# Optimization experiments

Measured on AMD Instinct MI355X. Metric: run time of the kernel, lower is better.

Reference implementation:

```python
import jax, jax.numpy as jnp
import numpy as np

N = 200000      # nodes
E = 1600000     # edges
B = 1000        # graphs
SD = 64         # state_dim
AD = 32         # action_dim
H = 128         # HIDDEN_LAYER
EPS = 1e-5


def setup_inputs() -> dict:
    key = jax.random.key(0)
    ks = jax.random.split(key, 16)
    x = jax.random.normal(ks[0], (N, SD), dtype=jnp.float32)
    action = jax.random.normal(ks[1], (N, AD), dtype=jnp.float32)
    edge_index = jax.random.randint(ks[2], (2, E), 0, N, dtype=jnp.int64)
    batch_size = jnp.sort(jax.random.randint(ks[3], (N,), 0, B, dtype=jnp.int64))
    # parameters (Linear weights stored [in, out]; torch init std=0.1 for fc layers)
    W_gcn = jax.random.normal(ks[4], (SD, H), dtype=jnp.float32) / np.sqrt(SD)
    b_gcn = jnp.zeros((H,), jnp.float32)
    g0 = jnp.ones((H,), jnp.float32); be0 = jnp.zeros((H,), jnp.float32)
    W1 = jax.random.normal(ks[5], (H, H), dtype=jnp.float32) * 0.1
    b1 = jnp.zeros((H,), jnp.float32)
    g1 = jnp.ones((H,), jnp.float32); be1 = jnp.zeros((H,), jnp.float32)
    W2 = jax.random.normal(ks[6], (AD, H), dtype=jnp.float32) * 0.1
    b2 = jnp.zeros((H,), jnp.float32)
    g2 = jnp.ones((H,), jnp.float32); be2 = jnp.zeros((H,), jnp.float32)
    W3 = jax.random.normal(ks[7], (2 * H, 1), dtype=jnp.float32) * 0.1
    b3 = jnp.zeros((1,), jnp.float32)
    return dict(x=x, action=action, W_gcn=W_gcn, b_gcn=b_gcn, g0=g0, be0=be0,
                W1=W1, b1=b1, g1=g1, be1=be1, W2=W2, b2=b2, g2=g2, be2=be2,
                W3=W3, b3=b3, edge_index=edge_index, batch_size=batch_size)


def _bn(h, gamma, beta):
    # BatchNorm1d, training-mode batch statistics over the node axis
    mu = jnp.mean(h, axis=0)
    var = jnp.var(h, axis=0)
    return (h - mu) * jax.lax.rsqrt(var + EPS) * gamma + beta


def _gcn(x, edge_index, W, b):
    # GCN conv with self-loops and symmetric normalization:
    # out_i = sum_{j in N(i) u {i}} (d_i d_j)^{-1/2} (x_j W) + b
    loops = jnp.arange(N, dtype=edge_index.dtype)
    src = jnp.concatenate([edge_index[0], loops])
    dst = jnp.concatenate([edge_index[1], loops])
    deg = jax.ops.segment_sum(jnp.ones_like(dst, dtype=x.dtype), dst, num_segments=N)
    dinv = jax.lax.rsqrt(deg)                       # deg >= 1 due to self-loops
    norm = dinv[src] * dinv[dst]                    # [E+N]
    xw = x @ W                                      # [N, H]
    msg = xw[src] * norm[:, None]                   # [E+N, H]
    return jax.ops.segment_sum(msg, dst, num_segments=N) + b


def reference(x, action, W_gcn, b_gcn, g0, be0, W1, b1, g1, be1,
              W2, b2, g2, be2, W3, b3, edge_index, batch_size):
    h0 = jax.nn.relu(_gcn(x, edge_index, W_gcn, b_gcn))
    h0n = _bn(h0, g0, be0)
    h1 = jax.nn.relu(h0n @ W1 + b1)
    h1n = _bn(h1, g1, be1)
    h2 = jax.nn.relu(action @ W2 + b2)
    h2n = _bn(h2, g2, be2)
    feat = jnp.concatenate([h1n, h2n], axis=1)      # [N, 2H]
    sums = jax.ops.segment_sum(feat, batch_size, num_segments=B)
    cnts = jax.ops.segment_sum(jnp.ones((N,), feat.dtype), batch_size, num_segments=B)
    pooled = sums / jnp.maximum(cnts, 1.0)[:, None]  # [B, 2H]
    return pooled @ W3 + b3                          # [B, 1]
```

## Files before the change

kernel.cpp:

```cpp
#include <hip/hip_runtime.h>

typedef unsigned short u16;
typedef unsigned int   u32;
typedef __bf16 bf16x8 __attribute__((ext_vector_type(8)));
typedef float  f32x4  __attribute__((ext_vector_type(4)));

#define EPS 1e-5f
#define BSHIFT 9

__device__ __forceinline__ float b2f(u16 u){ union{u32 i; float f;} v; v.i=((u32)u)<<16; return v.f; }
__device__ __forceinline__ u16 f2b(float f){
  u32 x = __float_as_uint(f);
  u32 r = x + 0x7fffu + ((x>>16)&1u);
  return (u16)(r>>16);
}

template<int K, bool RELU, bool HASBIAS, bool AF32, bool POOL>
__global__ __launch_bounds__(256) void k_gemm(const void* __restrict__ Av,
                                              const u16* __restrict__ BhiT,
                                              const u16* __restrict__ BloT,
                                              const float* __restrict__ bias,
                                              u16* __restrict__ C,
                                              float* __restrict__ stats,
                                              const int* __restrict__ batch,
                                              float* __restrict__ P, int M)
{
  constexpr int KM = K / 8;
  constexpr int KR = K / 32;
  __shared__ u16 lds[2 * 64 * K];
  __shared__ float sred[64], qred[64];
  const int tid = threadIdx.x;
  const int halfg = gridDim.x >> 1;
  const int ch = (blockIdx.x >= halfg) ? 1 : 0;
  const int t0 = blockIdx.x - ch * halfg;
  for (int i = tid; i < 64 * KM; i += 256) {
    const int n = i / KM, kb = i % KM;
    const int kb2 = kb ^ (n & (KM - 1));
    const int gsrc = ((ch * 64 + n) * KM + kb) * 8;
    *(uint4*)(&lds[(n * KM + kb2) * 8])          = *(const uint4*)(BhiT + gsrc);
    *(uint4*)(&lds[64 * K + (n * KM + kb2) * 8]) = *(const uint4*)(BloT + gsrc);
  }
  if (tid < 64) { sred[tid] = 0.f; qred[tid] = 0.f; }
  __syncthreads();
  const int wid = tid >> 6, lane = tid & 63, q = lane >> 4, r16 = lane & 15;
  const int nmt = (M + 127) >> 7;
  float ls[4], lq[4];
#pragma unroll
  for (int nb = 0; nb < 4; nb++) { ls[nb] = 0.f; lq[nb] = 0.f; }
  float bv[4];
#pragma unroll
  for (int nb = 0; nb < 4; nb++) bv[nb] = HASBIAS ? bias[ch * 64 + nb * 16 + r16] : 0.f;

  for (int mt = t0; mt < nmt; mt += halfg) {
    const int row0 = mt << 7;
    const bool ok1 = (row0 + 64) < M;

    bf16x8 av[2][KR];
    if (AF32) {
      const float* Af = (const float*)Av + (size_t)(row0 + (wid << 4) + r16) * K + q * 8;
#pragma unroll
      for (int kk = 0; kk < KR; kk++) {
        f32x4 x0 = *(const f32x4*)(Af + kk * 32);
        f32x4 x1 = *(const f32x4*)(Af + kk * 32 + 4);
#pragma unroll
        for (int j = 0; j < 4; j++) { av[0][kk][j] = (__bf16)x0[j]; av[0][kk][4 + j] = (__bf16)x1[j]; }
      }
      if (ok1) {
        const float* Ag = Af + (size_t)64 * K;
#pragma unroll
        for (int kk = 0; kk < KR; kk++) {
          f32x4 x0 = *(const f32x4*)(Ag + kk * 32);
          f32x4 x1 = *(const f32x4*)(Ag + kk * 32 + 4);
#pragma unroll
          for (int j = 0; j < 4; j++) { av[1][kk][j] = (__bf16)x0[j]; av[1][kk][4 + j] = (__bf16)x1[j]; }
        }
      }
    } else {
      const u16* Ab = (const u16*)Av + (size_t)(row0 + (wid << 4) + r16) * K + q * 8;
#pragma unroll
      for (int kk = 0; kk < KR; kk++) av[0][kk] = *(const bf16x8*)(Ab + kk * 32);
      if (ok1) {
#pragma unroll
        for (int kk = 0; kk < KR; kk++) av[1][kk] = *(const bf16x8*)(Ab + (size_t)64 * K + kk * 32);
      }
    }

    f32x4 acc[2][4];
#pragma unroll
    for (int rt = 0; rt < 2; rt++)
#pragma unroll
      for (int nb = 0; nb < 4; nb++) acc[rt][nb] = (f32x4){0.f, 0.f, 0.f, 0.f};
#pragma unroll
    for (int kk = 0; kk < KR; kk++) {
#pragma unroll
      for (int nb = 0; nb < 4; nb++) {
        const int n = nb * 16 + r16;
        const int kb2 = (kk * 4 + q) ^ (n & (KM - 1));
        const bf16x8 bh = *(const bf16x8*)(&lds[(n * KM + kb2) * 8]);
        const bf16x8 bl = *(const bf16x8*)(&lds[64 * K + (n * KM + kb2) * 8]);
        acc[0][nb] = __builtin_amdgcn_mfma_f32_16x16x32_bf16(av[0][kk], bh, acc[0][nb], 0, 0, 0);
        acc[0][nb] = __builtin_amdgcn_mfma_f32_16x16x32_bf16(av[0][kk], bl, acc[0][nb], 0, 0, 0);
        if (ok1) {
          acc[1][nb] = __builtin_amdgcn_mfma_f32_16x16x32_bf16(av[1][kk], bh, acc[1][nb], 0, 0, 0);
          acc[1][nb] = __builtin_amdgcn_mfma_f32_16x16x32_bf16(av[1][kk], bl, acc[1][nb], 0, 0, 0);
        }
      }
    }

#pragma unroll
    for (int rt = 0; rt < 2; rt++) {
      if (rt && !ok1) continue;
      const int rbase = row0 + rt * 64 + (wid << 4) + (q << 2);
#pragma unroll
      for (int nb = 0; nb < 4; nb++) {
        const int col = ch * 64 + nb * 16 + r16;
#pragma unroll
        for (int r = 0; r < 4; r++) {
          float v = acc[rt][nb][r] + bv[nb];
          if (RELU) v = fmaxf(v, 0.f);
          ls[nb] += v; lq[nb] += v * v;
          if (!POOL) C[(size_t)(rbase + r) * 128 + col] = f2b(v);
          else acc[rt][nb][r] = v;
        }
      }
      if (POOL) {
        int bg[4];
#pragma unroll
        for (int r = 0; r < 4; r++) bg[r] = batch[rbase + r];
        const int g0 = __shfl(bg[0], 0, 64);
        const int g1 = __shfl(bg[3], 48, 64);
        for (int g = g0; g <= g1; ++g) {
#pragma unroll
          for (int nb = 0; nb < 4; nb++) {
            float sv = 0.f;
#pragma unroll
            for (int r = 0; r < 4; r++) sv += (bg[r] == g) ? acc[rt][nb][r] : 0.f;
            sv += __shfl_xor(sv, 16, 64);
            sv += __shfl_xor(sv, 32, 64);
            if (q == 0) atomicAdd(&P[g * 128 + ch * 64 + nb * 16 + r16], sv);
          }
        }
      }
    }
  }
#pragma unroll
  for (int nb = 0; nb < 4; nb++) {
    atomicAdd(&sred[nb * 16 + r16], ls[nb]);
    atomicAdd(&qred[nb * 16 + r16], lq[nb]);
  }
  __syncthreads();
  if (tid < 64) {
    atomicAdd(&stats[ch * 64 + tid], sred[tid]);
    atomicAdd(&stats[128 + ch * 64 + tid], qred[tid]);
  }
}

__global__ void k_prep0(const float* __restrict__ Wg, const float* __restrict__ W2,
                        u16* __restrict__ WghiT, u16* __restrict__ WgloT,
                        u16* __restrict__ W2hiT, u16* __restrict__ W2loT,
                        const int* __restrict__ batch, int* __restrict__ gofs,
                        int* __restrict__ zbase, int zwords, int NZ, int N, int B)
{
  const int bid = blockIdx.x, t = threadIdx.x;
  if (bid < NZ) {
    const int i = bid * 2048 + t * 8;
    if (i < zwords) {
      *(int4*)(zbase + i)     = make_int4(0, 0, 0, 0);
      *(int4*)(zbase + i + 4) = make_int4(0, 0, 0, 0);
    }
  } else if (bid < NZ + 48) {
    const int i = (bid - NZ) * 256 + t;
    if (i < 64 * 128) {
      int k = i >> 7, n = i & 127;
      float w = Wg[i]; u16 h = f2b(w);
      WghiT[n * 64 + k] = h; WgloT[n * 64 + k] = f2b(w - b2f(h));
    } else if (i < 64 * 128 + 32 * 128) {
      int j = i - 64 * 128;
      int k = j >> 7, n = j & 127;
      float w = W2[j]; u16 h = f2b(w);
      W2hiT[n * 32 + k] = h; W2loT[n * 32 + k] = f2b(w - b2f(h));
    }
  } else {
    const int i = (bid - NZ - 48) * 256 + t;
    if (i == 0) { for (int g = 0; g <= batch[0]; g++) gofs[g] = 0; }
    if (i == N - 1) { for (int g = batch[N - 1] + 1; g <= B; g++) gofs[g] = N; }
    if (i < N - 1) {
      const int b0 = batch[i], b1 = batch[i + 1];
      for (int g = b0 + 1; g <= b1; g++) gofs[g] = i + 1;
    }
  }
}

__global__ __launch_bounds__(256) void k_bincnt(const int* __restrict__ dst, int* __restrict__ btot,
                                                int E, int NB)
{
  extern __shared__ int hist[];
  const int tid = threadIdx.x;
  for (int i = tid; i < NB; i += 256) hist[i] = 0;
  __syncthreads();
  const int chunk = (E + gridDim.x - 1) / gridDim.x;
  const int start = blockIdx.x * chunk;
  const int end = min(start + chunk, E);
  for (int e = start + tid; e < end; e += 256) atomicAdd(&hist[((u32)dst[e]) >> BSHIFT], 1);
  __syncthreads();
  for (int i = tid; i < NB; i += 256) if (hist[i]) atomicAdd(&btot[i], hist[i]);
}

__global__ void k_exscan(const int* __restrict__ in, int* __restrict__ out, int n)
{
  __shared__ int s[256];
  const int t = threadIdx.x;
  const int per = (n + 255) / 256;
  const int base = t * per;
  int loc[8]; int sum = 0;
  for (int j = 0; j < per; j++) { int v = (base + j < n) ? in[base + j] : 0; loc[j] = sum; sum += v; }
  s[t] = sum; __syncthreads();
  for (int o = 1; o < 256; o <<= 1) {
    int x = (t >= o) ? s[t - o] : 0;
    __syncthreads();
    s[t] += x;
    __syncthreads();
  }
  const int ex = s[t] - sum;
  for (int j = 0; j < per; j++) if (base + j < n) out[base + j] = ex + loc[j];
  if (t == 255) out[n] = s[255];
}

__global__ __launch_bounds__(256) void k_bin(const int* __restrict__ src, const int* __restrict__ dst,
                                             const int* __restrict__ bbase, int* __restrict__ bcur,
                                             uint2* __restrict__ pairs, int E, int NB)
{
  extern __shared__ int lds[];
  int* hist = lds; int* wbase = lds + NB;
  const int tid = threadIdx.x;
  for (int i = tid; i < NB; i += 256) hist[i] = 0;
  __syncthreads();
  const int chunk = (E + gridDim.x - 1) / gridDim.x;
  const int start = blockIdx.x * chunk;
  const int end = min(start + chunk, E);
  for (int e = start + tid; e < end; e += 256) atomicAdd(&hist[((u32)dst[e]) >> BSHIFT], 1);
  __syncthreads();
  for (int i = tid; i < NB; i += 256) {
    int c = hist[i];
    wbase[i] = c ? bbase[i] + atomicAdd(&bcur[i], c) : 0;
    hist[i] = 0;
  }
  __syncthreads();
  for (int e = start + tid; e < end; e += 256) {
    const int d = dst[e];
    const int b = ((u32)d) >> BSHIFT;
    const int o = atomicAdd(&hist[b], 1);
    pairs[wbase[b] + o] = make_uint2((u32)d, (u32)src[e]);
  }
}

__global__ __launch_bounds__(256) void k_bucket(const uint2* __restrict__ pairs,
                                                const int* __restrict__ bbase,
                                                const float* __restrict__ x,
                                                int* __restrict__ offsets, float* __restrict__ dinv,
                                                int* __restrict__ elist, u16* __restrict__ y,
                                                int N, int NB, int Etot)
{
  __shared__ int hist[512];
  __shared__ int scan[256];
  __shared__ int lcur[512];
  __shared__ float sdinv[512];
  const int b = blockIdx.x, t = threadIdx.x;
  const int nbase = b << BSHIFT;
  const int nn = min(1 << BSHIFT, N - nbase);
  hist[t] = 0; hist[256 + t] = 0;
  __syncthreads();
  const int p0 = bbase[b], p1 = bbase[b + 1];
  for (int p = p0 + t; p < p1; p += 256) atomicAdd(&hist[pairs[p].x - nbase], 1);
  __syncthreads();
  const int h0 = hist[2 * t], h1 = hist[2 * t + 1];
  const int psum = h0 + h1;
  scan[t] = psum; __syncthreads();
  for (int o = 1; o < 256; o <<= 1) {
    int xx = (t >= o) ? scan[t - o] : 0;
    __syncthreads();
    scan[t] += xx;
    __syncthreads();
  }
  const int ex = scan[t] - psum;
  const int li0 = 2 * t, li1 = 2 * t + 1;
  if (li0 < nn) {
    const int i = nbase + li0;
    const int off = p0 + ex + i;
    const float d = rsqrtf((float)(h0 + 1));
    offsets[i] = off; elist[off] = i; lcur[li0] = off + 1;
    dinv[i] = d; sdinv[li0] = d;
  }
  if (li1 < nn) {
    const int i = nbase + li1;
    const int off = p0 + ex + h0 + i;
    const float d = rsqrtf((float)(h1 + 1));
    offsets[i] = off; elist[off] = i; lcur[li1] = off + 1;
    dinv[i] = d; sdinv[li1] = d;
  }
  if (b == NB - 1 && t == 0) offsets[N] = Etot;
  __syncthreads();
  for (int p = p0 + t; p < p1; p += 256) {
    const uint2 pr = pairs[p];
    const int pos = atomicAdd(&lcur[pr.x - nbase], 1);
    elist[pos] = (int)pr.y;
  }
  const size_t ebase = (size_t)nbase * 64;
  const int total = nn * 64;
  for (int i = t * 8; i < total; i += 256 * 8) {
    const float d = sdinv[i >> 6];
    f32x4 a = *(const f32x4*)(x + ebase + i);
    f32x4 c = *(const f32x4*)(x + ebase + i + 4);
    u16 o[8];
#pragma unroll
    for (int j = 0; j < 4; j++) { o[j] = f2b(a[j] * d); o[4 + j] = f2b(c[j] * d); }
    *(uint4*)(y + ebase + i) = *(uint4*)o;
  }
}

__global__ __launch_bounds__(256) void k_agg(const u16* __restrict__ y, const int* __restrict__ offsets,
                                             const int* __restrict__ elist, const float* __restrict__ dinv,
                                             u16* __restrict__ aggx, int n)
{
  const int lane = threadIdx.x & 63;
  const int half = lane >> 5, l32 = lane & 31;
  const int g4 = l32 >> 3, sub = lane & 7;
  const int wid  = (blockIdx.x * 256 + threadIdx.x) >> 6;
  const int nw   = gridDim.x * 4;
  const int npair = (n + 1) >> 1;
  for (int pr = wid; pr < npair; pr += nw) {
    const int node = pr * 2 + half;
    const int s0 = offsets[node], s1 = offsets[node + 1];
    const int mydeg = s1 - s0;
    const int degA = __shfl(mydeg, 0, 64);
    const int degB = __shfl(mydeg, 32, 64);
    const int degmax = max(degA, degB);
    float a[8];
#pragma unroll
    for (int t = 0; t < 8; t++) a[t] = 0.f;
    for (int base = 0; base < degmax; base += 32) {
      const int m = mydeg - base;
      const int ev = (base + l32 < mydeg) ? elist[s0 + base + l32] : 0;
      const int iters = (min(32, degmax - base) + 3) >> 2;
      for (int it = 0; it < iters; it++) {
        const int j = it * 4 + g4;
        const int idx = __shfl(ev, half * 32 + j, 64);
        if (j < m) {
          const uint4 v = *(const uint4*)(y + (size_t)idx * 64 + sub * 8);
          const u32 w[4] = {v.x, v.y, v.z, v.w};
#pragma unroll
          for (int t = 0; t < 4; t++) {
            a[2 * t]     += b2f((u16)w[t]);
            a[2 * t + 1] += b2f((u16)(w[t] >> 16));
          }
        }
      }
    }
#pragma unroll
    for (int t = 0; t < 8; t++) {
      a[t] += __shfl_xor(a[t], 8, 64);
      a[t] += __shfl_xor(a[t], 16, 64);
    }
    if (g4 == 0) {
      const float di = dinv[node];
      u16 o[8];
#pragma unroll
      for (int t = 0; t < 8; t++) o[t] = f2b(a[t] * di);
      *(uint4*)(aggx + (size_t)node * 64 + sub * 8) = *(uint4*)o;
    }
  }
}

__global__ void k_prep1(const float* __restrict__ stats0, const float* __restrict__ W1,
                        const float* __restrict__ b1, const float* __restrict__ g0,
                        const float* __restrict__ be0, u16* __restrict__ W1hiT,
                        u16* __restrict__ W1loT, float* __restrict__ b1p, float n)
{
  __shared__ float A[8], Csh[8];
  const int t = threadIdx.x;
  if (t < 8) {
    const int k = blockIdx.x * 8 + t;
    const float mu = stats0[k] / n;
    const float var = fmaxf(stats0[128 + k] / n - mu * mu, 0.f);
    const float a = g0[k] * rsqrtf(var + EPS);
    A[t] = a; Csh[t] = be0[k] - mu * a;
  }
  __syncthreads();
  float acc = (blockIdx.x == 0) ? b1[t] : 0.f;
#pragma unroll
  for (int kk = 0; kk < 8; kk++) {
    const int k = blockIdx.x * 8 + kk;
    const float w0 = W1[k * 128 + t];
    acc += Csh[kk] * w0;
    const float w = A[kk] * w0;
    const u16 h = f2b(w);
    W1hiT[t * 128 + k] = h;
    W1loT[t * 128 + k] = f2b(w - b2f(h));
  }
  atomicAdd(&b1p[t], acc);
}

__global__ void k_prep2(const float* __restrict__ stats1, const float* __restrict__ stats2,
                        const float* __restrict__ g1, const float* __restrict__ be1,
                        const float* __restrict__ g2, const float* __restrict__ be2,
                        const float* __restrict__ W3, const float* __restrict__ b3,
                        float* __restrict__ w1f, float* __restrict__ w2f,
                        float* __restrict__ constS, float n)
{
  __shared__ float red[256];
  const int t = threadIdx.x;
  float c, wv;
  if (t < 128) {
    const float mu = stats1[t] / n;
    const float var = fmaxf(stats1[128 + t] / n - mu * mu, 0.f);
    const float a = g1[t] * rsqrtf(var + EPS);
    c = be1[t] - mu * a;
    wv = W3[t];
    w1f[t] = a * wv;
  } else {
    const int f = t - 128;
    const float mu = stats2[f] / n;
    const float var = fmaxf(stats2[128 + f] / n - mu * mu, 0.f);
    const float a = g2[f] * rsqrtf(var + EPS);
    c = be2[f] - mu * a;
    wv = W3[t];
    w2f[f] = a * wv;
  }
  red[t] = c * wv; __syncthreads();
  for (int o = 128; o; o >>= 1) { if (t < o) red[t] += red[t + o]; __syncthreads(); }
  if (t == 0) { constS[0] = red[0] + b3[0]; constS[1] = b3[0]; }
}

__global__ void k_out2(const float* __restrict__ P1, const float* __restrict__ P2,
                       const int* __restrict__ gofs, const float* __restrict__ w1f,
                       const float* __restrict__ w2f, const float* __restrict__ constS,
                       float* __restrict__ out, int B)
{
  const int lane = threadIdx.x & 63;
  const int g = (blockIdx.x * 256 + threadIdx.x) >> 6;
  if (g >= B) return;
  const int c = gofs[g + 1] - gofs[g];
  const int k = 2 * lane;
  float d = P1[g * 128 + k] * w1f[k] + P1[g * 128 + k + 1] * w1f[k + 1]
          + P2[g * 128 + k] * w2f[k] + P2[g * 128 + k + 1] * w2f[k + 1];
#pragma unroll
  for (int o = 1; o < 64; o <<= 1) d += __shfl_xor(d, o, 64);
  if (lane == 0) out[g] = (c > 0) ? d / (float)c + constS[0] : constS[1];
}

extern "C" void kernel_launch(void* const* d_in, const int* in_sizes, int n_in,
                              void* d_out, int out_size, void* d_ws, size_t ws_size,
                              hipStream_t stream)
{
  const float* x    = (const float*)d_in[0];
  const float* act  = (const float*)d_in[1];
  const float* Wg   = (const float*)d_in[2];
  const float* bg   = (const float*)d_in[3];
  const float* g0   = (const float*)d_in[4];
  const float* be0  = (const float*)d_in[5];
  const float* W1   = (const float*)d_in[6];
  const float* b1   = (const float*)d_in[7];
  const float* g1   = (const float*)d_in[8];
  const float* be1  = (const float*)d_in[9];
  const float* W2   = (const float*)d_in[10];
  const float* b2   = (const float*)d_in[11];
  const float* g2   = (const float*)d_in[12];
  const float* be2  = (const float*)d_in[13];
  const float* W3   = (const float*)d_in[14];
  const float* b3   = (const float*)d_in[15];
  const int* eidx   = (const int*)d_in[16];
  const int* batch  = (const int*)d_in[17];

  const int N = in_sizes[17];
  const int E = in_sizes[16] / 2;
  const int B = out_size;
  const int* src = eidx;
  const int* dst = eidx + E;
  const int NB = (N + (1 << BSHIFT) - 1) >> BSHIFT;

  char* ws = (char*)d_ws;
  size_t off = 0;
  auto alloc = [&](size_t bytes) -> char* {
    off = (off + 255) & ~(size_t)255;
    char* p = ws + off; off += bytes; return p;
  };

  u16* bufA = (u16*)alloc((size_t)N * 128 * 2);
  u16* xb   = (u16*)alloc((size_t)N * 64 * 2);
  u16* aggx = (u16*)alloc((size_t)N * 64 * 2);

  int zwords = 768 + 128 + 2 * NB + 2 * 128 * B;
  zwords = (zwords + 7) & ~7;
  char* zbase   = alloc((size_t)zwords * 4);
  float* stats0 = (float*)zbase;
  float* stats1 = stats0 + 256;
  float* stats2 = stats1 + 256;
  float* b1p    = stats2 + 256;
  int*   btot   = (int*)(b1p + 128);
  int*   bcur   = btot + NB;
  float* P1     = (float*)(bcur + NB);
  float* P2     = P1 + 128 * B;

  int*   offsets = (int*)alloc((size_t)(N + 1) * 4);
  float* dinv    = (float*)alloc((size_t)N * 4);
  int*   elist   = (int*)alloc((size_t)(E + N) * 4);
  uint2* pairs   = (uint2*)alloc((size_t)E * 8);
  int*   bbase   = (int*)alloc((size_t)(NB + 1) * 4);
  int*   gofs    = (int*)alloc((size_t)(B + 1) * 4);
  u16*   WghiT   = (u16*)alloc(128 * 64 * 2);
  u16*   WgloT   = (u16*)alloc(128 * 64 * 2);
  u16*   W1hiT   = (u16*)alloc(128 * 128 * 2);
  u16*   W1loT   = (u16*)alloc(128 * 128 * 2);
  u16*   W2hiT   = (u16*)alloc(128 * 32 * 2);
  u16*   W2loT   = (u16*)alloc(128 * 32 * 2);
  float* w1f     = (float*)alloc(128 * 4);
  float* w2f     = (float*)alloc(128 * 4);
  float* constS  = (float*)alloc(2 * 4);

  u16* h0 = bufA;

  const int NZ = (zwords + 2047) / 2048;
  const int nbounds = (N + 255) / 256;
  k_prep0<<<NZ + 48 + nbounds, 256, 0, stream>>>(Wg, W2, WghiT, WgloT, W2hiT, W2loT,
                                                 batch, gofs, (int*)zbase, zwords, NZ, N, B);
  k_bincnt<<<256, 256, NB * 4, stream>>>(dst, btot, E, NB);
  k_exscan<<<1, 256, 0, stream>>>(btot, bbase, NB);
  k_bin<<<256, 256, 2 * NB * 4, stream>>>(src, dst, bbase, bcur, pairs, E, NB);
  k_bucket<<<NB, 256, 0, stream>>>(pairs, bbase, x, offsets, dinv, elist, xb, N, NB, E + N);
  k_agg<<<2048, 256, 0, stream>>>(xb, offsets, elist, dinv, aggx, N);
  k_gemm<64, true, true, false, false><<<1024, 256, 0, stream>>>(aggx, WghiT, WgloT, bg,
                                                                 h0, stats0, nullptr, nullptr, N);
  k_prep1<<<16, 128, 0, stream>>>(stats0, W1, b1, g0, be0, W1hiT, W1loT, b1p, (float)N);
  k_gemm<128, true, true, false, true><<<1024, 256, 0, stream>>>(h0, W1hiT, W1loT, b1p,
                                                                 nullptr, stats1, batch, P1, N);
  k_gemm<32, true, true, true, true><<<1024, 256, 0, stream>>>(act, W2hiT, W2loT, b2,
                                                               nullptr, stats2, batch, P2, N);
  k_prep2<<<1, 256, 0, stream>>>(stats1, stats2, g1, be1, g2, be2, W3, b3, w1f, w2f, constS, (float)N);
  k_out2<<<(B * 64 + 255) / 256, 256, 0, stream>>>(P1, P2, gofs, w1f, w2f, constS, (float*)d_out, B);
}
```

Before: 397.1 us.

## Merge the two pooling GEMMs into one launch and fuse prep2 into output

Moves the GEMM body into a device function that uses dynamic shared memory, so a combined kernel can run the K=128 hidden GEMM and the K=32 action GEMM as disjoint block ranges of a single launch. It also folds the BatchNorm-to-W3 folding kernel into the final output kernel, which recomputes the scale factors per block in shared memory. Grid sizes change from 1024 to 768 and 512 blocks. This removes two launches and lets the two independent GEMMs share the GPU. In exchange the K=32 blocks reserve the larger K=128 shared-memory size, which may limit occupancy, and every output block repeats the small reduction.

```diff
diff --git a/kernel.cpp b/kernel.cpp
--- a/kernel.cpp
+++ b/kernel.cpp
@@ -16,23 +16,25 @@
 }
 
 template<int K, bool RELU, bool HASBIAS, bool AF32, bool POOL>
-__global__ __launch_bounds__(256) void k_gemm(const void* __restrict__ Av,
-                                              const u16* __restrict__ BhiT,
-                                              const u16* __restrict__ BloT,
-                                              const float* __restrict__ bias,
-                                              u16* __restrict__ C,
-                                              float* __restrict__ stats,
-                                              const int* __restrict__ batch,
-                                              float* __restrict__ P, int M)
+__device__ __forceinline__ void gemm_body(const void* __restrict__ Av,
+                                          const u16* __restrict__ BhiT,
+                                          const u16* __restrict__ BloT,
+                                          const float* __restrict__ bias,
+                                          u16* __restrict__ C,
+                                          float* __restrict__ stats,
+                                          const int* __restrict__ batch,
+                                          float* __restrict__ P, int M,
+                                          int bid, int halfg)
 {
   constexpr int KM = K / 8;
   constexpr int KR = K / 32;
-  __shared__ u16 lds[2 * 64 * K];
-  __shared__ float sred[64], qred[64];
+  extern __shared__ char smem[];
+  u16* lds    = (u16*)smem;
+  float* sred = (float*)(smem + (size_t)2 * 64 * K * 2);
+  float* qred = sred + 64;
   const int tid = threadIdx.x;
-  const int halfg = gridDim.x >> 1;
-  const int ch = (blockIdx.x >= halfg) ? 1 : 0;
-  const int t0 = blockIdx.x - ch * halfg;
+  const int ch = (bid >= halfg) ? 1 : 0;
+  const int t0 = bid - ch * halfg;
   for (int i = tid; i < 64 * KM; i += 256) {
     const int n = i / KM, kb = i % KM;
     const int kb2 = kb ^ (n & (KM - 1));
@@ -153,6 +155,43 @@
     atomicAdd(&stats[ch * 64 + tid], sred[tid]);
     atomicAdd(&stats[128 + ch * 64 + tid], qred[tid]);
   }
+}
+
+template<int K, bool RELU, bool HASBIAS, bool AF32, bool POOL>
+__global__ __launch_bounds__(256) void k_gemm(const void* __restrict__ Av,
+                                              const u16* __restrict__ BhiT,
+                                              const u16* __restrict__ BloT,
+                                              const float* __restrict__ bias,
+                                              u16* __restrict__ C,
+                                              float* __restrict__ stats,
+                                              const int* __restrict__ batch,
+                                              float* __restrict__ P, int M)
+{
+  gemm_body<K, RELU, HASBIAS, AF32, POOL>(Av, BhiT, BloT, bias, C, stats, batch, P, M,
+                                          blockIdx.x, gridDim.x >> 1);
+}
+
+__global__ __launch_bounds__(256) void k_gemm2(const void* __restrict__ A1,
+                                               const u16* __restrict__ B1hi,
+                                               const u16* __restrict__ B1lo,
+                                               const float* __restrict__ bias1,
+                                               float* __restrict__ stats1,
+                                               float* __restrict__ P1,
+                                               const void* __restrict__ A2,
+                                               const u16* __restrict__ B2hi,
+                                               const u16* __restrict__ B2lo,
+                                               const float* __restrict__ bias2,
+                                               float* __restrict__ stats2,
+                                               float* __restrict__ P2,
+                                               const int* __restrict__ batch,
+                                               int M, int g1blk, int g2blk)
+{
+  if ((int)blockIdx.x < g1blk)
+    gemm_body<128, true, true, false, true>(A1, B1hi, B1lo, bias1, nullptr, stats1,
+                                            batch, P1, M, blockIdx.x, g1blk >> 1);
+  else
+    gemm_body<32, true, true, true, true>(A2, B2hi, B2lo, bias2, nullptr, stats2,
+                                          batch, P2, M, blockIdx.x - g1blk, g2blk >> 1);
 }
 
 __global__ void k_prep0(const float* __restrict__ Wg, const float* __restrict__ W2,
@@ -400,14 +439,15 @@
   atomicAdd(&b1p[t], acc);
 }
 
-__global__ void k_prep2(const float* __restrict__ stats1, const float* __restrict__ stats2,
-                        const float* __restrict__ g1, const float* __restrict__ be1,
-                        const float* __restrict__ g2, const float* __restrict__ be2,
-                        const float* __restrict__ W3, const float* __restrict__ b3,
-                        float* __restrict__ w1f, float* __restrict__ w2f,
-                        float* __restrict__ constS, float n)
-{
-  __shared__ float red[256];
+__global__ void k_out3(const float* __restrict__ P1, const float* __restrict__ P2,
+                       const int* __restrict__ gofs,
+                       const float* __restrict__ stats1, const float* __restrict__ stats2,
+                       const float* __restrict__ g1, const float* __restrict__ be1,
+                       const float* __restrict__ g2, const float* __restrict__ be2,
+                       const float* __restrict__ W3, const float* __restrict__ b3,
+                       float* __restrict__ out, int B, float n)
+{
+  __shared__ float w1s[128], w2s[128], red[256], cS[2];
   const int t = threadIdx.x;
   float c, wv;
   if (t < 128) {
@@ -416,7 +456,7 @@
     const float a = g1[t] * rsqrtf(var + EPS);
     c = be1[t] - mu * a;
     wv = W3[t];
-    w1f[t] = a * wv;
+    w1s[t] = a * wv;
   } else {
     const int f = t - 128;
     const float mu = stats2[f] / n;
@@ -424,28 +464,22 @@
     const float a = g2[f] * rsqrtf(var + EPS);
     c = be2[f] - mu * a;
     wv = W3[t];
-    w2f[f] = a * wv;
+    w2s[f] = a * wv;
   }
   red[t] = c * wv; __syncthreads();
   for (int o = 128; o; o >>= 1) { if (t < o) red[t] += red[t + o]; __syncthreads(); }
-  if (t == 0) { constS[0] = red[0] + b3[0]; constS[1] = b3[0]; }
-}
-
-__global__ void k_out2(const float* __restrict__ P1, const float* __restrict__ P2,
-                       const int* __restrict__ gofs, const float* __restrict__ w1f,
-                       const float* __restrict__ w2f, const float* __restrict__ constS,
-                       float* __restrict__ out, int B)
-{
-  const int lane = threadIdx.x & 63;
-  const int g = (blockIdx.x * 256 + threadIdx.x) >> 6;
+  if (t == 0) { cS[0] = red[0] + b3[0]; cS[1] = b3[0]; }
+  __syncthreads();
+  const int lane = t & 63;
+  const int g = (blockIdx.x * 256 + t) >> 6;
   if (g >= B) return;
-  const int c = gofs[g + 1] - gofs[g];
+  const int cnt = gofs[g + 1] - gofs[g];
   const int k = 2 * lane;
-  float d = P1[g * 128 + k] * w1f[k] + P1[g * 128 + k + 1] * w1f[k + 1]
-          + P2[g * 128 + k] * w2f[k] + P2[g * 128 + k + 1] * w2f[k + 1];
+  float d = P1[g * 128 + k] * w1s[k] + P1[g * 128 + k + 1] * w1s[k + 1]
+          + P2[g * 128 + k] * w2s[k] + P2[g * 128 + k + 1] * w2s[k + 1];
 #pragma unroll
   for (int o = 1; o < 64; o <<= 1) d += __shfl_xor(d, o, 64);
-  if (lane == 0) out[g] = (c > 0) ? d / (float)c + constS[0] : constS[1];
+  if (lane == 0) out[g] = (cnt > 0) ? d / (float)cnt + cS[0] : cS[1];
 }
 
 extern "C" void kernel_launch(void* const* d_in, const int* in_sizes, int n_in,
@@ -513,11 +547,11 @@
   u16*   W1loT   = (u16*)alloc(128 * 128 * 2);
   u16*   W2hiT   = (u16*)alloc(128 * 32 * 2);
   u16*   W2loT   = (u16*)alloc(128 * 32 * 2);
-  float* w1f     = (float*)alloc(128 * 4);
-  float* w2f     = (float*)alloc(128 * 4);
-  float* constS  = (float*)alloc(2 * 4);
 
   u16* h0 = bufA;
+
+  const int smem64  = 2 * 64 * 64 * 2 + 512;
+  const int smem128 = 2 * 64 * 128 * 2 + 512;
 
   const int NZ = (zwords + 2047) / 2048;
   const int nbounds = (N + 255) / 256;
@@ -528,13 +562,13 @@
   k_bin<<<256, 256, 2 * NB * 4, stream>>>(src, dst, bbase, bcur, pairs, E, NB);
   k_bucket<<<NB, 256, 0, stream>>>(pairs, bbase, x, offsets, dinv, elist, xb, N, NB, E + N);
   k_agg<<<2048, 256, 0, stream>>>(xb, offsets, elist, dinv, aggx, N);
-  k_gemm<64, true, true, false, false><<<1024, 256, 0, stream>>>(aggx, WghiT, WgloT, bg,
-                                                                 h0, stats0, nullptr, nullptr, N);
+  k_gemm<64, true, true, false, false><<<768, 256, smem64, stream>>>(aggx, WghiT, WgloT, bg,
+                                                                     h0, stats0, nullptr, nullptr, N);
   k_prep1<<<16, 128, 0, stream>>>(stats0, W1, b1, g0, be0, W1hiT, W1loT, b1p, (float)N);
-  k_gemm<128, true, true, false, true><<<1024, 256, 0, stream>>>(h0, W1hiT, W1loT, b1p,
-                                                                 nullptr, stats1, batch, P1, N);
-  k_gemm<32, true, true, true, true><<<1024, 256, 0, stream>>>(act, W2hiT, W2loT, b2,
-                                                               nullptr, stats2, batch, P2, N);
-  k_prep2<<<1, 256, 0, stream>>>(stats1, stats2, g1, be1, g2, be2, W3, b3, w1f, w2f, constS, (float)N);
-  k_out2<<<(B * 64 + 255) / 256, 256, 0, stream>>>(P1, P2, gofs, w1f, w2f, constS, (float*)d_out, B);
-}
+  k_gemm2<<<768 + 512, 256, smem128, stream>>>(h0, W1hiT, W1loT, b1p, stats1, P1,
+                                               act, W2hiT, W2loT, b2, stats2, P2,
+                                               batch, N, 768, 512);
+  k_out3<<<(B * 64 + 255) / 256, 256, 0, stream>>>(P1, P2, gofs, stats1, stats2,
+                                                   g1, be1, g2, be2, W3, b3,
+                                                   (float*)d_out, B, (float)N);
+}
```

Measured after the change: 372.1 us. 6.3% less time.
